# Kernel optimization log

Measured on AMD Instinct MI355X. Metric: run time of the kernel, lower is better.

## Reference

```python
import jax, jax.numpy as jnp
import numpy as np

B, IN_F, NQ, L = 4096, 1024, 4, 2   # batch, in_features, qubits/circuit, entangler layers
C = IN_F // NQ                      # n_circuits = 256


def _rx(theta):
    # RX(theta) = [[cos(t/2), -i sin(t/2)], [-i sin(t/2), cos(t/2)]]
    c = jnp.cos(theta / 2).astype(jnp.complex64)
    s = jnp.sin(theta / 2).astype(jnp.complex64)
    return jnp.stack([jnp.stack([c, -1j * s]), jnp.stack([-1j * s, c])])


def _apply_1q(U, state, q):
    # contract 2x2 gate along qubit axis q of state with shape (2,)*NQ
    return jnp.moveaxis(jnp.tensordot(U, state, axes=([1], [q])), 0, q)


def _cnot(state, ctrl, tgt):
    s0 = jnp.take(state, 0, axis=ctrl)
    s1 = jnp.take(state, 1, axis=ctrl)
    t = tgt - 1 if tgt > ctrl else tgt
    s1 = jnp.flip(s1, axis=t)          # X on target in the ctrl=1 block
    return jnp.stack([s0, s1], axis=ctrl)


def _sim_one(xv, w):
    # xv: (NQ,) input angles; w: (L, NQ) variational angles
    # Angle embedding: RX(x_q) on |0> per qubit -> product state [cos, -i sin]
    cos = jnp.cos(xv / 2).astype(jnp.complex64)
    sin = (-1j) * jnp.sin(xv / 2).astype(jnp.complex64)
    state = jnp.stack([cos[0], sin[0]])
    for q in range(1, NQ):
        state = jnp.tensordot(state, jnp.stack([cos[q], sin[q]]), axes=0)
    # BasicEntanglerLayers: per layer, RX on each wire then ring of CNOTs
    for l in range(L):
        for q in range(NQ):
            state = _apply_1q(_rx(w[l, q]), state, q)
        for q in range(NQ):
            state = _cnot(state, q, (q + 1) % NQ)
    # Measurement: <Z_q> for every wire
    probs = jnp.real(state * jnp.conj(state))
    zsign = jnp.array([1.0, -1.0], jnp.float32)
    zs = [probs.sum(axis=tuple(a for a in range(NQ) if a != q)) @ zsign
          for q in range(NQ)]
    return jnp.stack(zs)


def setup_inputs() -> dict:
    key = jax.random.key(0)
    kx, kw = jax.random.split(key)
    x = jax.random.normal(kx, (B, IN_F), jnp.float32)
    weights = jax.random.uniform(kw, (C, L, NQ), jnp.float32, 0.0, 2.0 * np.pi)
    return {"x": x, "weights": weights}


def reference(x, weights):
    xr = x.reshape(B, C, NQ)
    sim = jax.vmap(jax.vmap(_sim_one, in_axes=(0, 0)), in_axes=(0, None))
    out = sim(xr, weights)                 # (B, C, NQ)
    return out.reshape(B, C * NQ).astype(jnp.float32)
```

## Files before the change

kernel.cpp:

```cpp
#include <hip/hip_runtime.h>
#include <math.h>


#define BQ 4096
#define CQ 256

__global__ __launch_bounds__(256) void qsim_kernel(
    const float* __restrict__ x,
    const float* __restrict__ w,
    float* __restrict__ out)
{
    const int tid = blockIdx.x * blockDim.x + threadIdx.x;
    const int c = tid & (CQ - 1);

    const float4 xv = reinterpret_cast<const float4*>(x)[tid];
    const float4 w0 = reinterpret_cast<const float4*>(w)[c * 2 + 0];
    const float4 w1 = reinterpret_cast<const float4*>(w)[c * 2 + 1];

    const float t0 = (xv.x + w0.x) * 0.5f;
    const float t1 = (xv.y + w0.y) * 0.5f;
    const float t2 = (xv.z + w0.z) * 0.5f;
    const float t3 = (xv.w + w0.w) * 0.5f;
    const float cA = __cosf(t0), sA = __sinf(t0);
    const float cB = __cosf(t1), sB = __sinf(t1);
    const float cC = __cosf(t2), sC = __sinf(t2);
    const float cD = __cosf(t3), sD = __sinf(t3);

    float gc[4], gs[4];
    gc[0] = __cosf(w1.x * 0.5f); gs[0] = __sinf(w1.x * 0.5f);
    gc[1] = __cosf(w1.y * 0.5f); gs[1] = __sinf(w1.y * 0.5f);
    gc[2] = __cosf(w1.z * 0.5f); gs[2] = __sinf(w1.z * 0.5f);
    gc[3] = __cosf(w1.w * 0.5f); gs[3] = __sinf(w1.w * 0.5f);

    float a01[4], a23[4];
    a01[0] = cA * cB; a01[1] = cA * sB; a01[2] = sA * cB; a01[3] = sA * sB;
    a23[0] = cC * cD; a23[1] = cC * sD; a23[2] = sC * cD; a23[3] = sC * sD;

    float m[16];
#pragma unroll
    for (int n = 0; n < 16; ++n) m[n] = a01[n >> 2] * a23[n & 3];

    constexpr int sp[16]   = {0,13,3,14,6,11,5,8,12,1,15,2,10,7,9,4};
    constexpr int phi1[16] = {0,1, 2,1, 2,1, 2,3, 2, 3,0, 3,2, 1,2,3};

    float ar[16], ai[16];
#pragma unroll
    for (int n = 0; n < 16; ++n) {
        const float r = m[sp[n]];
        ar[n] = (phi1[n] == 0) ? r : ((phi1[n] == 2) ? -r : 0.0f);
        ai[n] = (phi1[n] == 1) ? r : ((phi1[n] == 3) ? -r : 0.0f);
    }

    constexpr int gq[4]  = {3, 0, 1, 2};
    constexpr int gm[4]  = {1, 8, 4, 2};
#pragma unroll
    for (int g = 0; g < 4; ++g) {
        const float cg = gc[gq[g]], sg = gs[gq[g]];
        const int mk = gm[g];
#pragma unroll
        for (int n = 0; n < 16; ++n) {
            if (!(n & mk)) {
                const int n1 = n | mk;
                const float r0 = ar[n],  i0 = ai[n];
                const float r1 = ar[n1], i1 = ai[n1];
                ar[n]  = cg * r0 + sg * i1;
                ai[n]  = cg * i0 - sg * r1;
                ar[n1] = cg * r1 + sg * i0;
                ai[n1] = cg * i1 - sg * r0;
            }
        }
    }

    float p[16];
#pragma unroll
    for (int n = 0; n < 16; ++n) p[n] = ar[n] * ar[n] + ai[n] * ai[n];

    float sAv[8], dAv[8];
#pragma unroll
    for (int k = 0; k < 8; ++k) {
        sAv[k] = p[2 * k] + p[2 * k + 1];
        dAv[k] = p[2 * k] - p[2 * k + 1];
    }
    float dd[4], ss[4], sd[4];
#pragma unroll
    for (int j = 0; j < 4; ++j) {
        dd[j] = dAv[2 * j] - dAv[2 * j + 1];
        ss[j] = sAv[2 * j] + sAv[2 * j + 1];
        sd[j] = sAv[2 * j] - sAv[2 * j + 1];
    }
    const float g0 = dd[0] - dd[1], g1 = dd[2] - dd[3];
    const float u0 = ss[0] - ss[1], u1 = ss[2] - ss[3];
    const float v0 = sd[0] - sd[1], v1 = sd[2] - sd[3];

    const float z0 = g0 + g1;
    const float z3 = g0 - g1;
    const float z1 = u0 - u1;
    const float z2 = v0 - v1;

    reinterpret_cast<float4*>(out)[tid] = make_float4(z0, z1, z2, z3);
}

extern "C" void kernel_launch(void* const* d_in, const int* in_sizes, int n_in,
                              void* d_out, int out_size, void* d_ws, size_t ws_size,
                              hipStream_t stream) {
    const float* x = (const float*)d_in[0];
    const float* w = (const float*)d_in[1];
    float* out = (float*)d_out;

    const int total = BQ * CQ;
    qsim_kernel<<<total / 256, 256, 0, stream>>>(x, w, out);
}
```

Baseline: 77.49 us.

## Replace statevector simulation with closed-form expectation values

Swaps the explicit 16-amplitude complex statevector evolution and probability reductions for closed-form trigonometric product expressions for each <Z_q>, using full angles instead of half-angles. It also takes the circuit index straight from threadIdx.x, which only works because the block size equals the circuit count. The aim is to cut ALU work and register pressure in a kernel that is mostly memory bound. The risk is the correctness of the hand-derived algebra and slightly different rounding.

```diff
diff --git a/kernel.cpp b/kernel.cpp
--- a/kernel.cpp
+++ b/kernel.cpp
@@ -11,91 +11,36 @@
     float* __restrict__ out)
 {
     const int tid = blockIdx.x * blockDim.x + threadIdx.x;
-    const int c = tid & (CQ - 1);
+    const int c = threadIdx.x;
 
     const float4 xv = reinterpret_cast<const float4*>(x)[tid];
     const float4 w0 = reinterpret_cast<const float4*>(w)[c * 2 + 0];
     const float4 w1 = reinterpret_cast<const float4*>(w)[c * 2 + 1];
 
-    const float t0 = (xv.x + w0.x) * 0.5f;
-    const float t1 = (xv.y + w0.y) * 0.5f;
-    const float t2 = (xv.z + w0.z) * 0.5f;
-    const float t3 = (xv.w + w0.w) * 0.5f;
-    const float cA = __cosf(t0), sA = __sinf(t0);
-    const float cB = __cosf(t1), sB = __sinf(t1);
-    const float cC = __cosf(t2), sC = __sinf(t2);
-    const float cD = __cosf(t3), sD = __sinf(t3);
+    const float a0 = xv.x + w0.x;
+    const float a1 = xv.y + w0.y;
+    const float a2 = xv.z + w0.z;
+    const float a3 = xv.w + w0.w;
 
-    float gc[4], gs[4];
-    gc[0] = __cosf(w1.x * 0.5f); gs[0] = __sinf(w1.x * 0.5f);
-    gc[1] = __cosf(w1.y * 0.5f); gs[1] = __sinf(w1.y * 0.5f);
-    gc[2] = __cosf(w1.z * 0.5f); gs[2] = __sinf(w1.z * 0.5f);
-    gc[3] = __cosf(w1.w * 0.5f); gs[3] = __sinf(w1.w * 0.5f);
+    const float C0 = __cosf(a0), S0 = __sinf(a0);
+    const float C1 = __cosf(a1), S1 = __sinf(a1);
+    const float C2 = __cosf(a2), S2 = __sinf(a2);
+    const float C3 = __cosf(a3), S3 = __sinf(a3);
 
-    float a01[4], a23[4];
-    a01[0] = cA * cB; a01[1] = cA * sB; a01[2] = sA * cB; a01[3] = sA * sB;
-    a23[0] = cC * cD; a23[1] = cC * sD; a23[2] = sC * cD; a23[3] = sC * sD;
+    const float c0 = __cosf(w1.x), s0 = __sinf(w1.x);
+    const float c1 = __cosf(w1.y), s1 = __sinf(w1.y);
+    const float c2 = __cosf(w1.z), s2 = __sinf(w1.z);
+    const float c3 = __cosf(w1.w), s3 = __sinf(w1.w);
 
-    float m[16];
-#pragma unroll
-    for (int n = 0; n < 16; ++n) m[n] = a01[n >> 2] * a23[n & 3];
+    const float c1c2 = c1 * c2, s1s2 = s1 * s2;
+    const float U = C1 * C3, V = S1 * S3;
+    const float P = C0 * c3, Q = S0 * s3;
 
-    constexpr int sp[16]   = {0,13,3,14,6,11,5,8,12,1,15,2,10,7,9,4};
-    constexpr int phi1[16] = {0,1, 2,1, 2,1, 2,3, 2, 3,0, 3,2, 1,2,3};
-
-    float ar[16], ai[16];
-#pragma unroll
-    for (int n = 0; n < 16; ++n) {
-        const float r = m[sp[n]];
-        ar[n] = (phi1[n] == 0) ? r : ((phi1[n] == 2) ? -r : 0.0f);
-        ai[n] = (phi1[n] == 1) ? r : ((phi1[n] == 3) ? -r : 0.0f);
-    }
-
-    constexpr int gq[4]  = {3, 0, 1, 2};
-    constexpr int gm[4]  = {1, 8, 4, 2};
-#pragma unroll
-    for (int g = 0; g < 4; ++g) {
-        const float cg = gc[gq[g]], sg = gs[gq[g]];
-        const int mk = gm[g];
-#pragma unroll
-        for (int n = 0; n < 16; ++n) {
-            if (!(n & mk)) {
-                const int n1 = n | mk;
-                const float r0 = ar[n],  i0 = ai[n];
-                const float r1 = ar[n1], i1 = ai[n1];
-                ar[n]  = cg * r0 + sg * i1;
-                ai[n]  = cg * i0 - sg * r1;
-                ar[n1] = cg * r1 + sg * i0;
-                ai[n1] = cg * i1 - sg * r0;
-            }
-        }
-    }
-
-    float p[16];
-#pragma unroll
-    for (int n = 0; n < 16; ++n) p[n] = ar[n] * ar[n] + ai[n] * ai[n];
-
-    float sAv[8], dAv[8];
-#pragma unroll
-    for (int k = 0; k < 8; ++k) {
-        sAv[k] = p[2 * k] + p[2 * k + 1];
-        dAv[k] = p[2 * k] - p[2 * k + 1];
-    }
-    float dd[4], ss[4], sd[4];
-#pragma unroll
-    for (int j = 0; j < 4; ++j) {
-        dd[j] = dAv[2 * j] - dAv[2 * j + 1];
-        ss[j] = sAv[2 * j] + sAv[2 * j + 1];
-        sd[j] = sAv[2 * j] - sAv[2 * j + 1];
-    }
-    const float g0 = dd[0] - dd[1], g1 = dd[2] - dd[3];
-    const float u0 = ss[0] - ss[1], u1 = ss[2] - ss[3];
-    const float v0 = sd[0] - sd[1], v1 = sd[2] - sd[3];
-
-    const float z0 = g0 + g1;
-    const float z3 = g0 - g1;
-    const float z1 = u0 - u1;
-    const float z2 = v0 - v1;
+    const float z0 = fmaf(c1c2, fmaf(P, U, Q * V), s1s2 * fmaf(P, V, Q * U));
+    const float z1 = C3 * fmaf(c0 * c1, C0 * C2, (s0 * s1) * (S0 * S2));
+    const float z2 = c0 * fmaf(c1c2, U, s1s2 * V);
+    const float E = c0 * C2, F = s0 * S2, G = c2 * c3, H = s2 * s3;
+    const float z3 = fmaf(c1 * C0, fmaf(E, G, F * H), (s1 * S0) * fmaf(E, H, F * G));
 
     reinterpret_cast<float4*>(out)[tid] = make_float4(z0, z1, z2, z3);
 }
```

Result: faster. 69.36 us (median of 2 runs) (-10.5%).
